# Kernel tuning notes

Hardware: AMD Instinct MI355X
Metric: run time of the kernel (lower is better)

Reference implementation:

```python
import jax, jax.numpy as jnp
import numpy as np

NUM_HEADS = 8
T = 8  # hardcoded temporal dim in the original forward
MD = 3  # max_displacement -> 7x7 window
EPS = 1e-12  # F.normalize eps


def l2_normalize(x, axis):
    n = jnp.sqrt(jnp.sum(x * x, axis=axis, keepdims=True))
    return x / jnp.maximum(n, EPS)


def correlation_7x7(q, k):
    # q, k: [B, C, H, W]; FlowNet-style correlation, kernel_size=1, max_disp=3.
    # out[b, u, v, h, w] = sum_c q[b,c,h,w] * k[b,c,h+u-3,w+v-3] (zero padded)
    B, C, H, W = q.shape
    kp = jnp.pad(k, ((0, 0), (0, 0), (MD, MD), (MD, MD)))
    outs = []
    for dy in range(2 * MD + 1):
        for dx in range(2 * MD + 1):
            ks = kp[:, :, dy:dy + H, dx:dx + W]
            outs.append(jnp.sum(q * ks, axis=1))  # [B, H, W]
    corr = jnp.stack(outs, axis=1)  # [B, 49, H, W]
    return corr.reshape(B, 2 * MD + 1, 2 * MD + 1, H, W)


def setup_inputs() -> dict:
    key = jax.random.key(0)
    ks = jax.random.split(key, 6)
    B, N, C = 8, 8192, 256
    hd = C // NUM_HEADS
    std = 0.02
    return {
        "x": jax.random.normal(ks[0], (B, N, C), dtype=jnp.float32),
        "w_qk": jax.random.normal(ks[1], (2 * C, C), dtype=jnp.float32) * std,
        "w_corr": jax.random.normal(ks[2], (hd, 49), dtype=jnp.float32) * std,
        "b_corr": jnp.zeros((hd,), dtype=jnp.float32),
        "w_proj": jax.random.normal(ks[3], (C, C), dtype=jnp.float32) * std,
        "b_proj": jnp.zeros((C,), dtype=jnp.float32),
    }


def reference(x, w_qk, w_corr, b_corr, w_proj, b_proj):
    B, N, C = x.shape
    nh = NUM_HEADS
    hd = C // nh
    H = int(np.sqrt(N // T))
    W = H

    # qk projection (no bias): [B, N, 2C] -> q, k each [B, nh, N, hd]
    qk = jnp.einsum('bnc,dc->bnd', x, w_qk)
    qk = qk.reshape(B, N, 2, nh, hd).transpose(2, 0, 3, 1, 4)
    q, k = qk[0], qk[1]

    # 'b n (t h w) d -> (b n) t d h w'
    q = q.reshape(B * nh, T, H, W, hd).transpose(0, 1, 4, 2, 3)
    k = k.reshape(B * nh, T, H, W, hd).transpose(0, 1, 4, 2, 3)

    # temporal postfix: k[t+1], last frame repeated
    k_post = jnp.concatenate([k[:, 1:], k[:, -1:]], axis=1)

    qp = q.reshape(B * nh * T, hd, H, W)
    kp = k_post.reshape(B * nh * T, hd, H, W)
    qp = l2_normalize(qp, axis=1)
    kp = l2_normalize(kp, axis=1)

    corr = correlation_7x7(qp, kp)  # [(B nh T), 7, 7, H, W]
    # 'b u v h w -> b (h w) (u v)'
    corr = corr.transpose(0, 3, 4, 1, 2).reshape(B * nh * T, H * W, 49)

    v = jnp.einsum('bpk,dk->bpd', corr, w_corr) + b_corr  # [(B nh T), HW, hd]

    # '(b n t) (h w) d -> b n (t h w) d' then 'b h n d -> b n (h d)'
    out = v.reshape(B, nh, T * H * W, hd).transpose(0, 2, 1, 3).reshape(B, N, C)
    out = jnp.einsum('bnc,dc->bnd', out, w_proj) + b_proj
    return out
```

## Files before the change

kernel.cpp:

```cpp
#include <hip/hip_runtime.h>

typedef _Float16 half8 __attribute__((ext_vector_type(8)));
typedef _Float16 half2v __attribute__((ext_vector_type(2)));
typedef float float4v __attribute__((ext_vector_type(4)));

__device__ __forceinline__ float hmul_acc(unsigned a, unsigned b, float c) {
  half2v ha = __builtin_bit_cast(half2v, a);
  half2v hb = __builtin_bit_cast(half2v, b);
  c += (float)ha[0] * (float)hb[0];
  c += (float)ha[1] * (float)hb[1];
  return c;
}
__device__ __forceinline__ unsigned hscale(unsigned a, float s) {
  half2v ha = __builtin_bit_cast(half2v, a);
  half2v r;
  r[0] = (_Float16)((float)ha[0] * s);
  r[1] = (_Float16)((float)ha[1] * s);
  return __builtin_bit_cast(unsigned, r);
}

__global__ void cvt_f2h(const float4* __restrict__ s, ushort4* __restrict__ d, int n4) {
  int i = blockIdx.x * 256 + threadIdx.x;
  if (i < n4) {
    float4 v = s[i];
    _Float16 a = (_Float16)v.x, b = (_Float16)v.y, c = (_Float16)v.z, e = (_Float16)v.w;
    ushort4 o;
    o.x = __builtin_bit_cast(unsigned short, a);
    o.y = __builtin_bit_cast(unsigned short, b);
    o.z = __builtin_bit_cast(unsigned short, c);
    o.w = __builtin_bit_cast(unsigned short, e);
    d[i] = o;
  }
}

__global__ __launch_bounds__(256, 2)
void gemm_qk(const _Float16* __restrict__ A, const _Float16* __restrict__ Bw,
             _Float16* __restrict__ qo, _Float16* __restrict__ ko) {
  __shared__ uint4 Ash[512];
  __shared__ uint4 Bsh[512];
  const int tid = threadIdx.x;
  const int lane = tid & 63, w = tid >> 6;
  const int wm = w >> 1, wn = w & 1;
  const int ml = lane & 15, qd = lane >> 4;
  const int m0 = blockIdx.y * 128, n0 = blockIdx.x * 128;

  float4v acc[4][4];
  float4v z = {0.f, 0.f, 0.f, 0.f};
#pragma unroll
  for (int i = 0; i < 4; ++i)
#pragma unroll
    for (int j = 0; j < 4; ++j) acc[i][j] = z;

  const _Float16* Ap = A + (size_t)m0 * 256;
  const _Float16* Bp = Bw + (size_t)n0 * 256;

  for (int kt = 0; kt < 8; ++kt) {
    int k0 = kt * 32;
#pragma unroll
    for (int i = 0; i < 2; ++i) {
      int g = tid + i * 256;
      int row = g >> 2, kb = g & 3;
      uint4 va = *(const uint4*)(Ap + row * 256 + k0 + kb * 8);
      uint4 vb = *(const uint4*)(Bp + row * 256 + k0 + kb * 8);
      int slot = (row << 2) | (kb ^ ((row >> 1) & 3));
      Ash[slot] = va;
      Bsh[slot] = vb;
    }
    __syncthreads();
    half8 af[4], bf[4];
#pragma unroll
    for (int im = 0; im < 4; ++im) {
      int rowA = wm * 64 + im * 16 + ml;
      int sA = (rowA << 2) | (qd ^ ((rowA >> 1) & 3));
      af[im] = *(const half8*)((const _Float16*)Ash + sA * 8);
      int rowB = wn * 64 + im * 16 + ml;
      int sB = (rowB << 2) | (qd ^ ((rowB >> 1) & 3));
      bf[im] = *(const half8*)((const _Float16*)Bsh + sB * 8);
    }
#pragma unroll
    for (int im = 0; im < 4; ++im)
#pragma unroll
      for (int in = 0; in < 4; ++in)
        acc[im][in] = __builtin_amdgcn_mfma_f32_16x16x32_f16(af[im], bf[in], acc[im][in], 0, 0, 0);
    __syncthreads();
  }

#pragma unroll
  for (int im = 0; im < 4; ++im) {
    int rowr0 = m0 + wm * 64 + im * 16 + qd * 4;
#pragma unroll
    for (int in = 0; in < 4; ++in) {
      int col = n0 + wn * 64 + in * 16 + ml;
      int s = col >> 8, h = (col >> 5) & 7, j = col & 31;
      _Float16* dst = s ? ko : qo;
#pragma unroll
      for (int r = 0; r < 4; ++r) {
        int rowr = rowr0 + r;
        int b = rowr >> 13, n = rowr & 8191;
        int t = n >> 10, yx = n & 1023;
        int p = b * 64 + h * 8 + t;
        dst[((size_t)p * 1024 + yx) * 32 + j] = (_Float16)acc[im][in][r];
      }
    }
  }
}

__global__ __launch_bounds__(256, 2)
void corr_kernel(const _Float16* __restrict__ q16, const _Float16* __restrict__ k16,
                 const float* __restrict__ wcorr, const float* __restrict__ bcorr,
                 _Float16* __restrict__ outp) {
  __shared__ uint4 smem[2304];
  __shared__ uint4 wcs[288];
  __shared__ float bcs[32];

  const int tid = threadIdx.x;
  const int bx = blockIdx.x;
  const int p = bx >> 2, tile = bx & 3;
  const int y0 = (tile >> 1) * 16, x0 = (tile & 1) * 16;
  const int b = p >> 6, h = (p >> 3) & 7, t = p & 7;
  const int pk = (t < 7) ? p + 1 : p;
  const int ty = tid >> 4, tx = tid & 15;

  _Float16* wch = (_Float16*)wcs;
  for (int idx = tid; idx < 2304; idx += 256) {
    int d = idx / 72, kk = idx - d * 72;
    wch[idx] = (kk < 49) ? (_Float16)wcorr[d * 49 + kk] : (_Float16)0.f;
  }
  if (tid < 32) bcs[tid] = bcorr[tid];

  const _Float16* kbase = k16 + (size_t)pk * 32768;
#pragma unroll
  for (int i = 0; i < 8; ++i) {
    int g = tid + i * 256;
    if (g < 1936) {
      int vec = g >> 2, part = g & 3;
      int ky = vec / 22, kx = vec - ky * 22;
      int gy = y0 + ky - 3, gx = x0 + kx - 3;
      uint4 val = make_uint4(0u, 0u, 0u, 0u);
      if (gy >= 0 && gy < 32 && gx >= 0 && gx < 32)
        val = *(const uint4*)(kbase + ((size_t)gy * 32 + gx) * 32 + part * 8);
      int slot = (vec << 2) | (part ^ (vec & 3) ^ ((vec >> 2) & 3));
      smem[slot] = val;
    }
  }
  __syncthreads();

  for (int v = tid; v < 484; v += 256) {
    int base = v << 2;
    int sw = (v & 3) ^ ((v >> 2) & 3);
    uint4 gg[4];
#pragma unroll
    for (int pq = 0; pq < 4; ++pq) gg[pq] = smem[base | (pq ^ sw)];
    float ss = 0.f;
#pragma unroll
    for (int pq = 0; pq < 4; ++pq) {
      const unsigned* u = (const unsigned*)&gg[pq];
#pragma unroll
      for (int e = 0; e < 4; ++e) ss = hmul_acc(u[e], u[e], ss);
    }
    float sc = 1.f / fmaxf(sqrtf(ss), 1e-12f);
#pragma unroll
    for (int pq = 0; pq < 4; ++pq) {
      unsigned* u = (unsigned*)&gg[pq];
#pragma unroll
      for (int e = 0; e < 4; ++e) u[e] = hscale(u[e], sc);
      smem[base | (pq ^ sw)] = gg[pq];
    }
  }
  __syncthreads();

  const _Float16* qptr = q16 + (size_t)p * 32768 + ((size_t)(y0 + ty) * 32 + (x0 + tx)) * 32;
  uint4 qv[4];
#pragma unroll
  for (int i = 0; i < 4; ++i) qv[i] = *(const uint4*)(qptr + i * 8);
  const unsigned* qu = (const unsigned*)qv;
  float qss = 0.f;
#pragma unroll
  for (int e = 0; e < 16; ++e) qss = hmul_acc(qu[e], qu[e], qss);
  float qsc = 1.f / fmaxf(sqrtf(qss), 1e-12f);

  float corr[49];
#pragma unroll
  for (int dy = 0; dy < 7; ++dy) {
#pragma unroll
    for (int dx = 0; dx < 7; ++dx) {
      int vec = (ty + dy) * 22 + (tx + dx);
      int base = vec << 2;
      int sw = (vec & 3) ^ ((vec >> 2) & 3);
      float c = 0.f;
#pragma unroll
      for (int pq = 0; pq < 4; ++pq) {
        uint4 kk = smem[base | (pq ^ sw)];
        const unsigned* ku = (const unsigned*)&kk;
#pragma unroll
        for (int e = 0; e < 4; ++e) c = hmul_acc(qu[pq * 4 + e], ku[e], c);
      }
      corr[dy * 7 + dx] = c * qsc;
    }
  }
  __syncthreads();

  _Float16* corrm = (_Float16*)smem;
#pragma unroll
  for (int i = 0; i < 9; ++i) {
    uint4 val;
    unsigned* vu = (unsigned*)&val;
#pragma unroll
    for (int e = 0; e < 4; ++e) {
      int idx = i * 8 + e * 2;
      half2v hh;
      hh[0] = (_Float16)(idx < 49 ? corr[idx] : 0.f);
      hh[1] = (_Float16)(idx + 1 < 49 ? corr[idx + 1] : 0.f);
      vu[e] = __builtin_bit_cast(unsigned, hh);
    }
    smem[tid * 9 + i] = val;
  }
  __syncthreads();

  const int lane = tid & 63, w = tid >> 6;
  const int ml = lane & 15, qd = lane >> 4;
  float4v vacc[4][2];
  float4v z = {0.f, 0.f, 0.f, 0.f};
#pragma unroll
  for (int im = 0; im < 4; ++im) { vacc[im][0] = z; vacc[im][1] = z; }
#pragma unroll
  for (int ks = 0; ks < 2; ++ks) {
    half8 bfrag[2];
#pragma unroll
    for (int nt = 0; nt < 2; ++nt)
      bfrag[nt] = *(const half8*)(wch + (nt * 16 + ml) * 72 + ks * 32 + qd * 8);
#pragma unroll
    for (int im = 0; im < 4; ++im) {
      half8 afrag = *(const half8*)(corrm + (w * 64 + im * 16 + ml) * 72 + ks * 32 + qd * 8);
#pragma unroll
      for (int nt = 0; nt < 2; ++nt)
        vacc[im][nt] = __builtin_amdgcn_mfma_f32_16x16x32_f16(afrag, bfrag[nt], vacc[im][nt], 0, 0, 0);
    }
  }

#pragma unroll
  for (int im = 0; im < 4; ++im) {
#pragma unroll
    for (int nt = 0; nt < 2; ++nt) {
      int d = nt * 16 + ml;
      float bias = bcs[d];
#pragma unroll
      for (int r = 0; r < 4; ++r) {
        int pos = w * 64 + im * 16 + qd * 4 + r;
        int py = pos >> 4, px = pos & 15;
        int n = t * 1024 + (y0 + py) * 32 + (x0 + px);
        outp[(((size_t)b * 8192 + n) << 8) + h * 32 + d] = (_Float16)(vacc[im][nt][r] + bias);
      }
    }
  }
}

__global__ __launch_bounds__(256, 2)
void gemm_proj(const _Float16* __restrict__ A, const _Float16* __restrict__ Bw,
               const float* __restrict__ bp, float* __restrict__ out) {
  __shared__ uint4 Ash[512];
  __shared__ uint4 Bsh[512];
  const int tid = threadIdx.x;
  const int lane = tid & 63, w = tid >> 6;
  const int wm = w >> 1, wn = w & 1;
  const int ml = lane & 15, qd = lane >> 4;
  const int m0 = blockIdx.y * 128, n0 = blockIdx.x * 128;

  float4v acc[4][4];
  float4v z = {0.f, 0.f, 0.f, 0.f};
#pragma unroll
  for (int i = 0; i < 4; ++i)
#pragma unroll
    for (int j = 0; j < 4; ++j) acc[i][j] = z;

  const _Float16* Ap = A + (size_t)m0 * 256;
  const _Float16* Bp = Bw + (size_t)n0 * 256;

  for (int kt = 0; kt < 8; ++kt) {
    int k0 = kt * 32;
#pragma unroll
    for (int i = 0; i < 2; ++i) {
      int g = tid + i * 256;
      int row = g >> 2, kb = g & 3;
      uint4 va = *(const uint4*)(Ap + row * 256 + k0 + kb * 8);
      uint4 vb = *(const uint4*)(Bp + row * 256 + k0 + kb * 8);
      int slot = (row << 2) | (kb ^ ((row >> 1) & 3));
      Ash[slot] = va;
      Bsh[slot] = vb;
    }
    __syncthreads();
    half8 af[4], bf[4];
#pragma unroll
    for (int im = 0; im < 4; ++im) {
      int rowA = wm * 64 + im * 16 + ml;
      int sA = (rowA << 2) | (qd ^ ((rowA >> 1) & 3));
      af[im] = *(const half8*)((const _Float16*)Ash + sA * 8);
      int rowB = wn * 64 + im * 16 + ml;
      int sB = (rowB << 2) | (qd ^ ((rowB >> 1) & 3));
      bf[im] = *(const half8*)((const _Float16*)Bsh + sB * 8);
    }
#pragma unroll
    for (int im = 0; im < 4; ++im)
#pragma unroll
      for (int in = 0; in < 4; ++in)
        acc[im][in] = __builtin_amdgcn_mfma_f32_16x16x32_f16(af[im], bf[in], acc[im][in], 0, 0, 0);
    __syncthreads();
  }

#pragma unroll
  for (int im = 0; im < 4; ++im) {
    int rowr0 = m0 + wm * 64 + im * 16 + qd * 4;
#pragma unroll
    for (int in = 0; in < 4; ++in) {
      int col = n0 + wn * 64 + in * 16 + ml;
      float bias = bp[col];
#pragma unroll
      for (int r = 0; r < 4; ++r)
        out[(size_t)(rowr0 + r) * 256 + col] = acc[im][in][r] + bias;
    }
  }
}

extern "C" void kernel_launch(void* const* d_in, const int* in_sizes, int n_in,
                              void* d_out, int out_size, void* d_ws, size_t ws_size,
                              hipStream_t stream) {
  const float* x      = (const float*)d_in[0];
  const float* w_qk   = (const float*)d_in[1];
  const float* w_corr = (const float*)d_in[2];
  const float* b_corr = (const float*)d_in[3];
  const float* w_proj = (const float*)d_in[4];
  const float* b_proj = (const float*)d_in[5];
  float* out = (float*)d_out;

  char* ws = (char*)d_ws;
  _Float16* x16   = (_Float16*)(ws);
  _Float16* q16   = (_Float16*)(ws + 33554432);
  _Float16* k16   = (_Float16*)(ws + 67108864);
  _Float16* op16  = (_Float16*)(ws + 100663296);
  _Float16* wqk16 = (_Float16*)(ws + 134217728);
  _Float16* wpj16 = (_Float16*)(ws + 134479872);

  cvt_f2h<<<16384, 256, 0, stream>>>((const float4*)x, (ushort4*)x16, 4194304);
  cvt_f2h<<<128, 256, 0, stream>>>((const float4*)w_qk, (ushort4*)wqk16, 32768);
  cvt_f2h<<<64, 256, 0, stream>>>((const float4*)w_proj, (ushort4*)wpj16, 16384);
  gemm_qk<<<dim3(4, 512), 256, 0, stream>>>(x16, wqk16, q16, k16);
  corr_kernel<<<2048, 256, 0, stream>>>(q16, k16, w_corr, b_corr, op16);
  gemm_proj<<<dim3(2, 512), 256, 0, stream>>>(op16, wpj16, b_proj, out);
}
```

Before: 257.9 us.

## Use direct global-to-LDS loads in GEMMs, fdot2 in correlation, fold bias, fuse converts

Replaces the register-staged, swizzled LDS fills in both GEMMs with global_load_lds direct copies into an unswizzled layout. Switches correlation dot products to the fdot2 builtin and pre-scales q to drop a per-output multiply. Folds the correlation bias into the weight matrix through a constant-one column, and merges the three fp32-to-fp16 conversion launches into one. It also raises corr_kernel's occupancy hint. The unswizzled LDS layout risks bank conflicts on fragment reads, and there is still no double buffering.

```diff
diff --git a/kernel.cpp b/kernel.cpp
--- a/kernel.cpp
+++ b/kernel.cpp
@@ -4,12 +4,16 @@
 typedef _Float16 half2v __attribute__((ext_vector_type(2)));
 typedef float float4v __attribute__((ext_vector_type(4)));
 
-__device__ __forceinline__ float hmul_acc(unsigned a, unsigned b, float c) {
+__device__ __forceinline__ float dot2acc(unsigned a, unsigned b, float c) {
+#if __has_builtin(__builtin_amdgcn_fdot2)
+  return __builtin_amdgcn_fdot2(__builtin_bit_cast(half2v, a), __builtin_bit_cast(half2v, b), c, false);
+#else
   half2v ha = __builtin_bit_cast(half2v, a);
   half2v hb = __builtin_bit_cast(half2v, b);
   c += (float)ha[0] * (float)hb[0];
   c += (float)ha[1] * (float)hb[1];
   return c;
+#endif
 }
 __device__ __forceinline__ unsigned hscale(unsigned a, float s) {
   half2v ha = __builtin_bit_cast(half2v, a);
@@ -18,26 +22,37 @@
   r[1] = (_Float16)((float)ha[1] * s);
   return __builtin_bit_cast(unsigned, r);
 }
-
-__global__ void cvt_f2h(const float4* __restrict__ s, ushort4* __restrict__ d, int n4) {
-  int i = blockIdx.x * 256 + threadIdx.x;
-  if (i < n4) {
-    float4 v = s[i];
-    _Float16 a = (_Float16)v.x, b = (_Float16)v.y, c = (_Float16)v.z, e = (_Float16)v.w;
-    ushort4 o;
-    o.x = __builtin_bit_cast(unsigned short, a);
-    o.y = __builtin_bit_cast(unsigned short, b);
-    o.z = __builtin_bit_cast(unsigned short, c);
-    o.w = __builtin_bit_cast(unsigned short, e);
-    d[i] = o;
-  }
+__device__ __forceinline__ void gload_lds16(const void* g, void* l) {
+  __builtin_amdgcn_global_load_lds((const __attribute__((address_space(1))) unsigned*)g,
+                                   (__attribute__((address_space(3))) unsigned*)l, 16, 0, 0);
+}
+
+__global__ void cvt_all(const float4* __restrict__ x, const float4* __restrict__ wqk,
+                        const float4* __restrict__ wpj,
+                        ushort4* __restrict__ x16, ushort4* __restrict__ wqk16,
+                        ushort4* __restrict__ wpj16) {
+  int b = blockIdx.x;
+  const float4* s;
+  ushort4* d;
+  int i;
+  if (b < 16384) { s = x; d = x16; i = b * 256 + threadIdx.x; }
+  else if (b < 16512) { s = wqk; d = wqk16; i = (b - 16384) * 256 + threadIdx.x; }
+  else { s = wpj; d = wpj16; i = (b - 16512) * 256 + threadIdx.x; }
+  float4 v = s[i];
+  _Float16 a = (_Float16)v.x, bb = (_Float16)v.y, c = (_Float16)v.z, e = (_Float16)v.w;
+  ushort4 o;
+  o.x = __builtin_bit_cast(unsigned short, a);
+  o.y = __builtin_bit_cast(unsigned short, bb);
+  o.z = __builtin_bit_cast(unsigned short, c);
+  o.w = __builtin_bit_cast(unsigned short, e);
+  d[i] = o;
 }
 
 __global__ __launch_bounds__(256, 2)
 void gemm_qk(const _Float16* __restrict__ A, const _Float16* __restrict__ Bw,
              _Float16* __restrict__ qo, _Float16* __restrict__ ko) {
-  __shared__ uint4 Ash[512];
-  __shared__ uint4 Bsh[512];
+  __shared__ _Float16 Ash[4096];
+  __shared__ _Float16 Bsh[4096];
   const int tid = threadIdx.x;
   const int lane = tid & 63, w = tid >> 6;
   const int wm = w >> 1, wn = w & 1;
@@ -53,29 +68,21 @@
 
   const _Float16* Ap = A + (size_t)m0 * 256;
   const _Float16* Bp = Bw + (size_t)n0 * 256;
+  const int gr = w * 64 + lane;
+  const int row0 = gr >> 2, kb = gr & 3;
 
   for (int kt = 0; kt < 8; ++kt) {
     int k0 = kt * 32;
-#pragma unroll
-    for (int i = 0; i < 2; ++i) {
-      int g = tid + i * 256;
-      int row = g >> 2, kb = g & 3;
-      uint4 va = *(const uint4*)(Ap + row * 256 + k0 + kb * 8);
-      uint4 vb = *(const uint4*)(Bp + row * 256 + k0 + kb * 8);
-      int slot = (row << 2) | (kb ^ ((row >> 1) & 3));
-      Ash[slot] = va;
-      Bsh[slot] = vb;
-    }
+    gload_lds16(Ap + row0 * 256 + k0 + kb * 8, Ash + (size_t)(w * 64) * 8);
+    gload_lds16(Ap + (row0 + 64) * 256 + k0 + kb * 8, Ash + (size_t)(256 + w * 64) * 8);
+    gload_lds16(Bp + row0 * 256 + k0 + kb * 8, Bsh + (size_t)(w * 64) * 8);
+    gload_lds16(Bp + (row0 + 64) * 256 + k0 + kb * 8, Bsh + (size_t)(256 + w * 64) * 8);
     __syncthreads();
     half8 af[4], bf[4];
 #pragma unroll
     for (int im = 0; im < 4; ++im) {
-      int rowA = wm * 64 + im * 16 + ml;
-      int sA = (rowA << 2) | (qd ^ ((rowA >> 1) & 3));
-      af[im] = *(const half8*)((const _Float16*)Ash + sA * 8);
-      int rowB = wn * 64 + im * 16 + ml;
-      int sB = (rowB << 2) | (qd ^ ((rowB >> 1) & 3));
-      bf[im] = *(const half8*)((const _Float16*)Bsh + sB * 8);
+      af[im] = *(const half8*)(Ash + (wm * 64 + im * 16 + ml) * 32 + qd * 8);
+      bf[im] = *(const half8*)(Bsh + (wn * 64 + im * 16 + ml) * 32 + qd * 8);
     }
 #pragma unroll
     for (int im = 0; im < 4; ++im)
@@ -105,13 +112,12 @@
   }
 }
 
-__global__ __launch_bounds__(256, 2)
+__global__ __launch_bounds__(256, 4)
 void corr_kernel(const _Float16* __restrict__ q16, const _Float16* __restrict__ k16,
                  const float* __restrict__ wcorr, const float* __restrict__ bcorr,
                  _Float16* __restrict__ outp) {
   __shared__ uint4 smem[2304];
-  __shared__ uint4 wcs[288];
-  __shared__ float bcs[32];
+  __shared__ uint4 wcs[256];
 
   const int tid = threadIdx.x;
   const int bx = blockIdx.x;
@@ -122,11 +128,11 @@
   const int ty = tid >> 4, tx = tid & 15;
 
   _Float16* wch = (_Float16*)wcs;
-  for (int idx = tid; idx < 2304; idx += 256) {
-    int d = idx / 72, kk = idx - d * 72;
-    wch[idx] = (kk < 49) ? (_Float16)wcorr[d * 49 + kk] : (_Float16)0.f;
-  }
-  if (tid < 32) bcs[tid] = bcorr[tid];
+  for (int idx = tid; idx < 2048; idx += 256) {
+    int d = idx >> 6, kk = idx & 63;
+    float v = (kk < 49) ? wcorr[d * 49 + kk] : (kk == 49 ? bcorr[d] : 0.f);
+    wch[idx] = (_Float16)v;
+  }
 
   const _Float16* kbase = k16 + (size_t)pk * 32768;
 #pragma unroll
@@ -156,7 +162,7 @@
     for (int pq = 0; pq < 4; ++pq) {
       const unsigned* u = (const unsigned*)&gg[pq];
 #pragma unroll
-      for (int e = 0; e < 4; ++e) ss = hmul_acc(u[e], u[e], ss);
+      for (int e = 0; e < 4; ++e) ss = dot2acc(u[e], u[e], ss);
     }
     float sc = 1.f / fmaxf(sqrtf(ss), 1e-12f);
 #pragma unroll
@@ -173,11 +179,13 @@
   uint4 qv[4];
 #pragma unroll
   for (int i = 0; i < 4; ++i) qv[i] = *(const uint4*)(qptr + i * 8);
-  const unsigned* qu = (const unsigned*)qv;
+  unsigned* qu = (unsigned*)qv;
   float qss = 0.f;
 #pragma unroll
-  for (int e = 0; e < 16; ++e) qss = hmul_acc(qu[e], qu[e], qss);
+  for (int e = 0; e < 16; ++e) qss = dot2acc(qu[e], qu[e], qss);
   float qsc = 1.f / fmaxf(sqrtf(qss), 1e-12f);
+#pragma unroll
+  for (int e = 0; e < 16; ++e) qu[e] = hscale(qu[e], qsc);
 
   float corr[49];
 #pragma unroll
@@ -193,30 +201,30 @@
         uint4 kk = smem[base | (pq ^ sw)];
         const unsigned* ku = (const unsigned*)&kk;
 #pragma unroll
-        for (int e = 0; e < 4; ++e) c = hmul_acc(qu[pq * 4 + e], ku[e], c);
+        for (int e = 0; e < 4; ++e) c = dot2acc(qu[pq * 4 + e], ku[e], c);
       }
-      corr[dy * 7 + dx] = c * qsc;
+      corr[dy * 7 + dx] = c;
     }
   }
   __syncthreads();
 
-  _Float16* corrm = (_Float16*)smem;
-#pragma unroll
-  for (int i = 0; i < 9; ++i) {
+#pragma unroll
+  for (int i = 0; i < 8; ++i) {
     uint4 val;
     unsigned* vu = (unsigned*)&val;
 #pragma unroll
     for (int e = 0; e < 4; ++e) {
       int idx = i * 8 + e * 2;
       half2v hh;
-      hh[0] = (_Float16)(idx < 49 ? corr[idx] : 0.f);
-      hh[1] = (_Float16)(idx + 1 < 49 ? corr[idx + 1] : 0.f);
+      hh[0] = (_Float16)(idx < 49 ? corr[idx] : (idx == 49 ? 1.f : 0.f));
+      hh[1] = (_Float16)(idx + 1 < 49 ? corr[idx + 1] : (idx + 1 == 49 ? 1.f : 0.f));
       vu[e] = __builtin_bit_cast(unsigned, hh);
     }
     smem[tid * 9 + i] = val;
   }
   __syncthreads();
 
+  _Float16* corrm = (_Float16*)smem;
   const int lane = tid & 63, w = tid >> 6;
   const int ml = lane & 15, qd = lane >> 4;
   float4v vacc[4][2];
@@ -228,7 +236,7 @@
     half8 bfrag[2];
 #pragma unroll
     for (int nt = 0; nt < 2; ++nt)
-      bfrag[nt] = *(const half8*)(wch + (nt * 16 + ml) * 72 + ks * 32 + qd * 8);
+      bfrag[nt] = *(const half8*)(wch + (nt * 16 + ml) * 64 + ks * 32 + qd * 8);
 #pragma unroll
     for (int im = 0; im < 4; ++im) {
       half8 afrag = *(const half8*)(corrm + (w * 64 + im * 16 + ml) * 72 + ks * 32 + qd * 8);
@@ -243,13 +251,12 @@
 #pragma unroll
     for (int nt = 0; nt < 2; ++nt) {
       int d = nt * 16 + ml;
-      float bias = bcs[d];
 #pragma unroll
       for (int r = 0; r < 4; ++r) {
         int pos = w * 64 + im * 16 + qd * 4 + r;
         int py = pos >> 4, px = pos & 15;
         int n = t * 1024 + (y0 + py) * 32 + (x0 + px);
-        outp[(((size_t)b * 8192 + n) << 8) + h * 32 + d] = (_Float16)(vacc[im][nt][r] + bias);
+        outp[(((size_t)b * 8192 + n) << 8) + h * 32 + d] = (_Float16)vacc[im][nt][r];
       }
     }
   }
@@ -258,8 +265,8 @@
 __global__ __launch_bounds__(256, 2)
 void gemm_proj(const _Float16* __restrict__ A, const _Float16* __restrict__ Bw,
                const float* __restrict__ bp, float* __restrict__ out) {
-  __shared__ uint4 Ash[512];
-  __shared__ uint4 Bsh[512];
+  __shared__ _Float16 Ash[4096];
+  __shared__ _Float16 Bsh[4096];
   const int tid = threadIdx.x;
   const int lane = tid & 63, w = tid >> 6;
   const int wm = w >> 1, wn = w & 1;
@@ -275,29 +282,21 @@
 
   const _Float16* Ap = A + (size_t)m0 * 256;
   const _Float16* Bp = Bw + (size_t)n0 * 256;
+  const int gr = w * 64 + lane;
+  const int row0 = gr >> 2, kb = gr & 3;
 
   for (int kt = 0; kt < 8; ++kt) {
     int k0 = kt * 32;
-#pragma unroll
-    for (int i = 0; i < 2; ++i) {
-      int g = tid + i * 256;
-      int row = g >> 2, kb = g & 3;
-      uint4 va = *(const uint4*)(Ap + row * 256 + k0 + kb * 8);
-      uint4 vb = *(const uint4*)(Bp + row * 256 + k0 + kb * 8);
-      int slot = (row << 2) | (kb ^ ((row >> 1) & 3));
-      Ash[slot] = va;
-      Bsh[slot] = vb;
-    }
+    gload_lds16(Ap + row0 * 256 + k0 + kb * 8, Ash + (size_t)(w * 64) * 8);
+    gload_lds16(Ap + (row0 + 64) * 256 + k0 + kb * 8, Ash + (size_t)(256 + w * 64) * 8);
+    gload_lds16(Bp + row0 * 256 + k0 + kb * 8, Bsh + (size_t)(w * 64) * 8);
+    gload_lds16(Bp + (row0 + 64) * 256 + k0 + kb * 8, Bsh + (size_t)(256 + w * 64) * 8);
     __syncthreads();
     half8 af[4], bf[4];
 #pragma unroll
     for (int im = 0; im < 4; ++im) {
-      int rowA = wm * 64 + im * 16 + ml;
-      int sA = (rowA << 2) | (qd ^ ((rowA >> 1) & 3));
-      af[im] = *(const half8*)((const _Float16*)Ash + sA * 8);
-      int rowB = wn * 64 + im * 16 + ml;
-      int sB = (rowB << 2) | (qd ^ ((rowB >> 1) & 3));
-      bf[im] = *(const half8*)((const _Float16*)Bsh + sB * 8);
+      af[im] = *(const half8*)(Ash + (wm * 64 + im * 16 + ml) * 32 + qd * 8);
+      bf[im] = *(const half8*)(Bsh + (wn * 64 + im * 16 + ml) * 32 + qd * 8);
     }
 #pragma unroll
     for (int im = 0; im < 4; ++im)
@@ -340,9 +339,8 @@
   _Float16* wqk16 = (_Float16*)(ws + 134217728);
   _Float16* wpj16 = (_Float16*)(ws + 134479872);
 
-  cvt_f2h<<<16384, 256, 0, stream>>>((const float4*)x, (ushort4*)x16, 4194304);
-  cvt_f2h<<<128, 256, 0, stream>>>((const float4*)w_qk, (ushort4*)wqk16, 32768);
-  cvt_f2h<<<64, 256, 0, stream>>>((const float4*)w_proj, (ushort4*)wpj16, 16384);
+  cvt_all<<<16576, 256, 0, stream>>>((const float4*)x, (const float4*)w_qk, (const float4*)w_proj,
+                                     (ushort4*)x16, (ushort4*)wqk16, (ushort4*)wpj16);
   gemm_qk<<<dim3(4, 512), 256, 0, stream>>>(x16, wqk16, q16, k16);
   corr_kernel<<<2048, 256, 0, stream>>>(q16, k16, w_corr, b_corr, op16);
   gemm_proj<<<dim3(2, 512), 256, 0, stream>>>(op16, wpj16, b_proj, out);
```

Measured after the change: 235.0 us. 1.1x faster.
